# Kernel optimization log

Measured on AMD Instinct MI355X. Metric: run time of the kernel, lower is better.

## Reference

```python
import jax, jax.numpy as jnp
import numpy as np

B, T, C, H = 4096, 128, 128, 64  # T must equal BLOCK_SIZE=128, C=EMBEDDING_DIM=128


def setup_inputs() -> dict:
    key = jax.random.key(0)
    k1, k2, k3, k4, k5, k6 = jax.random.split(key, 6)
    source_embedding = jax.random.normal(k1, (B, T, C), dtype=jnp.float32)
    target_embedding = jax.random.normal(k2, (B, T, C), dtype=jnp.float32)
    # realistic padding: positions < length are valid; guarantees col 0 valid (no NaN rows)
    lengths = jax.random.randint(k3, (B,), 1, T + 1)
    pad_mask = jnp.arange(T)[None, :] < lengths[:, None]  # (B, T) bool
    Wq = jax.random.normal(k4, (C, H), dtype=jnp.float32) * 0.02
    Wk = jax.random.normal(k5, (C, H), dtype=jnp.float32) * 0.02
    Wv = jax.random.normal(k6, (C, H), dtype=jnp.float32) * 0.02
    return {"source_embedding": source_embedding, "target_embedding": target_embedding,
            "pad_mask": pad_mask, "Wq": Wq, "Wk": Wk, "Wv": Wv}


def reference(source_embedding, target_embedding, pad_mask, Wq, Wk, Wv):
    # q from target, k/v from source (cross-attention capable), bias-free projections
    q = target_embedding @ Wq   # (B, T, H)
    k = source_embedding @ Wk   # (B, T, H)
    v = source_embedding @ Wv   # (B, T, H)
    scale = k.shape[-1] ** -0.5
    wei = jnp.einsum('btd,bsd->bts', q, k) * scale  # (B, T, T)
    causal = jnp.tril(jnp.ones((T, T), dtype=bool))  # needs_future_mask=True
    mask = pad_mask[:, None, :] & causal[None, :, :]  # fuse pad + future masks
    wei = jnp.where(mask, wei, -jnp.inf)
    wei = jax.nn.softmax(wei, axis=-1)
    # dropout disabled (eval mode) for deterministic reference
    out = wei @ v  # (B, T, H)
    return out
```

## Files before the change

kernel.cpp:

```cpp
#include <hip/hip_runtime.h>
#include <stdint.h>


typedef uint32_t u32x2 __attribute__((ext_vector_type(2)));
typedef uint32_t u32x4 __attribute__((ext_vector_type(4)));
typedef float    f32x4 __attribute__((ext_vector_type(4)));
typedef __bf16   bf16x8 __attribute__((ext_vector_type(8)));

static __device__ __forceinline__ uint32_t pack2(float a, float b) {
  uint32_t ua = __builtin_bit_cast(uint32_t, a);
  uint32_t ub = __builtin_bit_cast(uint32_t, b);
  ua += 0x7FFFu + ((ua >> 16) & 1u);
  ub += 0x7FFFu + ((ub >> 16) & 1u);
  return (ua >> 16) | (ub & 0xFFFF0000u);
}
static __device__ __forceinline__ uint32_t cvt2(float a, float b) {
  uint16_t lo = __builtin_bit_cast(uint16_t, (__bf16)a);
  uint16_t hi = __builtin_bit_cast(uint16_t, (__bf16)b);
  return (uint32_t)lo | ((uint32_t)hi << 16);
}
static __device__ __forceinline__ f32x4 mfma16(u32x4 a, u32x4 b, f32x4 c) {
  return __builtin_amdgcn_mfma_f32_16x16x32_bf16(
      __builtin_bit_cast(bf16x8, a), __builtin_bit_cast(bf16x8, b), c, 0, 0, 0);
}

__global__ void prep_w(const float* __restrict__ Wq, const float* __restrict__ Wk,
                       const float* __restrict__ Wv, const void* __restrict__ mask,
                       uint32_t* __restrict__ ws) {
  const int blk = blockIdx.x;
  const int l = threadIdx.x;
  if (blk < 48) {
    const int m  = blk >> 4;
    const int ct = (blk >> 2) & 3;
    const int ks = blk & 3;
    const float* W = (m == 0) ? Wq : ((m == 1) ? Wk : Wv);
    const int h  = ct * 16 + (l & 15);
    const int c0 = ks * 32 + (l >> 4) * 8;
    u32x4 v;
#pragma unroll
    for (int p = 0; p < 4; ++p)
      v[p] = pack2(W[(c0 + 2 * p) * 64 + h], W[(c0 + 2 * p + 1) * 64 + h]);
    ((u32x4*)ws)[blk * 64 + l] = v;
  } else {
    const uint32_t* mw = (const uint32_t*)mask;
    int fl = 0;
    for (int i = l * 16; i < l * 16 + 16; ++i) {
      uint32_t x = mw[i];
      if (x == 0x3F800000u) fl = 2;
      else if (x > 1u && fl != 2) fl = 1;
    }
#pragma unroll
    for (int off = 32; off > 0; off >>= 1) {
      int o = __shfl_down(fl, off);
      fl = (o > fl) ? o : fl;
    }
    if (l == 0) ws[12288] = (uint32_t)fl;
  }
}

__global__ __launch_bounds__(512, 3) void attn_fused(
    const float* __restrict__ src, const float* __restrict__ tgt,
    const void* __restrict__ mask, const uint32_t* __restrict__ ws,
    float* __restrict__ out) {
  __shared__ __align__(16) uint8_t lds[49664];
  uint8_t* const EMB = lds;
  uint8_t* const Kb  = lds + 16384;
  uint8_t* const Vb  = lds + 32768;
  float*  const BIAS = (float*)(lds + 49152);

  const int b   = blockIdx.x;
  const int tid = (int)threadIdx.x;
  const int l   = tid & 63;
  const int w   = tid >> 6;
  const int l15 = l & 15;
  const int g4  = l >> 4;
  const int ct  = w & 3;
  const int sg  = (w >> 2) * 2;
  const int tq  = 16 * w + l15;

  const u32x4* wsv = (const u32x4*)ws;
  const int mflag = (int)ws[12288];
  const float* const srcb = src + (size_t)b * 16384;
  const float* const tgtb = tgt + (size_t)b * 16384;

  f32x4 qv[8];
  {
    const float* pq = tgtb + tq * 128 + g4 * 8;
#pragma unroll
    for (int ks = 0; ks < 4; ++ks) {
      qv[2 * ks]     = *(const f32x4*)(pq + ks * 32);
      qv[2 * ks + 1] = *(const f32x4*)(pq + ks * 32 + 4);
    }
  }
  f32x4 pf[4];
  auto stage_load = [&](const float* gbase) {
#pragma unroll
    for (int p = 0; p < 4; ++p)
      pf[p] = *(const f32x4*)(gbase + tid * 4 + p * 2048);
  };
  stage_load(srcb);
  float biasv = 0.0f;
  if (tid < 128) {
    bool valid;
    if (mflag == 1)      valid = ((const uint8_t*)mask)[b * 128 + tid] != 0;
    else if (mflag == 0) valid = ((const int*)mask)[b * 128 + tid] != 0;
    else                 valid = ((const float*)mask)[b * 128 + tid] != 0.0f;
    biasv = valid ? 0.0f : -1e30f;
  }

  uint32_t qp[8];
  {
    f32x4 c0 = {0,0,0,0}, c1 = {0,0,0,0}, c2 = {0,0,0,0}, c3 = {0,0,0,0};
#pragma unroll
    for (int ks = 0; ks < 4; ++ks) {
      u32x4 e = { cvt2(qv[2*ks][0], qv[2*ks][1]), cvt2(qv[2*ks][2], qv[2*ks][3]),
                  cvt2(qv[2*ks+1][0], qv[2*ks+1][1]), cvt2(qv[2*ks+1][2], qv[2*ks+1][3]) };
      c0 = mfma16(wsv[(0  + ks) * 64 + l], e, c0);
      c1 = mfma16(wsv[(4  + ks) * 64 + l], e, c1);
      c2 = mfma16(wsv[(8  + ks) * 64 + l], e, c2);
      c3 = mfma16(wsv[(12 + ks) * 64 + l], e, c3);
    }
    qp[0] = cvt2(c0[0], c0[1]); qp[1] = cvt2(c0[2], c0[3]);
    qp[2] = cvt2(c1[0], c1[1]); qp[3] = cvt2(c1[2], c1[3]);
    qp[4] = cvt2(c2[0], c2[1]); qp[5] = cvt2(c2[2], c2[3]);
    qp[6] = cvt2(c3[0], c3[1]); qp[7] = cvt2(c3[2], c3[3]);
  }

  auto stage_write = [&]() {
#pragma unroll
    for (int p = 0; p < 4; ++p) {
      const int c   = tid + p * 512;
      const int row = c >> 5;
      const int cc  = c & 31;
      u32x2 d = { cvt2(pf[p][0], pf[p][1]), cvt2(pf[p][2], pf[p][3]) };
      *(u32x2*)(EMB + (row << 8) + ((((cc >> 1) ^ (row & 7))) << 4) + ((cc & 1) << 3)) = d;
    }
  };
  u32x4 wk[4], wv[4];
#pragma unroll
  for (int ks = 0; ks < 4; ++ks) {
    wk[ks] = wsv[((4 + ct) * 4 + ks) * 64 + l];
    wv[ks] = wsv[((8 + ct) * 4 + ks) * 64 + l];
  }
  auto projKV = [&](int half) {
#pragma unroll
    for (int i = 0; i < 2; ++i) {
      const int st  = sg + i;
      const int row = st * 16 + l15;
      f32x4 cK = {0, 0, 0, 0}, cV = {0, 0, 0, 0};
#pragma unroll
      for (int ks = 0; ks < 4; ++ks) {
        u32x4 e = *(const u32x4*)(EMB + (row << 8) + ((((ks * 4 + g4) ^ (row & 7))) << 4));
        cK = mfma16(wk[ks], e, cK);
        cV = mfma16(e, wv[ks], cV);
      }
      const int s  = half * 64 + st * 16 + l15;
      const int h0 = ct * 16 + g4 * 4;
      u32x2 dk = { cvt2(cK[0], cK[1]), cvt2(cK[2], cK[3]) };
      *(u32x2*)(Kb + (s << 7) + ((((h0 >> 3) ^ (s & 7))) << 4) + ((h0 & 7) << 1)) = dk;
      const int s0 = half * 64 + st * 16 + g4 * 4;
      const int h  = ct * 16 + l15;
      u32x2 dv = { cvt2(cV[0], cV[1]), cvt2(cV[2], cV[3]) };
      *(u32x2*)(Vb + (h << 8) + ((((s0 >> 3) ^ (h & 7))) << 4) + ((s0 & 7) << 1)) = dv;
    }
  };

  stage_write();
  if (tid < 128) BIAS[tid] = biasv;
  __syncthreads();
  stage_load(srcb + 8192);
  projKV(0);
  __syncthreads();
  stage_write();
  __syncthreads();
  projKV(1);
  __syncthreads();

  uint8_t* const Qw = EMB + (w << 11) + (l15 << 7);
#pragma unroll
  for (int ctq = 0; ctq < 4; ++ctq) {
    u32x2 dq = { qp[2 * ctq], qp[2 * ctq + 1] };
    const int cw = ctq * 2 + (g4 >> 1);
    *(u32x2*)(Qw + (((cw ^ (l15 & 7))) << 4) + ((g4 & 1) << 3)) = dq;
  }
  u32x4 qB[2];
#pragma unroll
  for (int ks = 0; ks < 2; ++ks)
    qB[ks] = *(const u32x4*)(Qw + ((((ks * 4 + g4) ^ (l15 & 7))) << 4));

  f32x4 sacc[8];
#pragma unroll
  for (int mt = 0; mt < 8; ++mt) sacc[mt] = {0, 0, 0, 0};
  __builtin_amdgcn_s_setprio(1);
#pragma unroll
  for (int mt = 0; mt < 8; ++mt) {
    const int srow = mt * 16 + l15;
    u32x4 k0 = *(const u32x4*)(Kb + (srow << 7) + (((g4 ^ (srow & 7))) << 4));
    u32x4 k1 = *(const u32x4*)(Kb + (srow << 7) + ((((4 + g4) ^ (srow & 7))) << 4));
    sacc[mt] = mfma16(k0, qB[0], sacc[mt]);
    sacc[mt] = mfma16(k1, qB[1], sacc[mt]);
  }
  __builtin_amdgcn_s_setprio(0);

  __syncthreads();

  float m = -3.0e38f;
#pragma unroll
  for (int mt = 0; mt < 8; ++mt) {
    f32x4 b4 = *(const f32x4*)(BIAS + mt * 16 + g4 * 4);
#pragma unroll
    for (int r = 0; r < 4; ++r) {
      float v = sacc[mt][r] * 0.125f + b4[r];
      sacc[mt][r] = v;
      m = fmaxf(m, v);
    }
  }
  m = fmaxf(m, __shfl_xor(m, 16));
  m = fmaxf(m, __shfl_xor(m, 32));
  float sum = 0.0f;
#pragma unroll
  for (int mt = 0; mt < 8; ++mt) {
#pragma unroll
    for (int r = 0; r < 4; ++r) {
      const int s = mt * 16 + g4 * 4 + r;
      float p = __expf(sacc[mt][r] - m);
      p = (s <= tq) ? p : 0.0f;
      sacc[mt][r] = p;
      sum += p;
    }
  }
  sum += __shfl_xor(sum, 16);
  sum += __shfl_xor(sum, 32);
  const float inv = 1.0f / sum;

  uint8_t* const Pr = (l15 < 8) ? (EMB + (w << 11) + (l15 << 8))
                                : (Kb + (w << 11) + ((l15 - 8) << 8));
#pragma unroll
  for (int mt = 0; mt < 8; ++mt) {
    u32x2 d = { cvt2(sacc[mt][0], sacc[mt][1]), cvt2(sacc[mt][2], sacc[mt][3]) };
    const int c = mt * 2 + (g4 >> 1);
    *(u32x2*)(Pr + (((c ^ l15)) << 4) + ((g4 & 1) << 3)) = d;
  }

  f32x4 oacc[4];
#pragma unroll
  for (int vt = 0; vt < 4; ++vt) oacc[vt] = {0, 0, 0, 0};
  __builtin_amdgcn_s_setprio(1);
#pragma unroll
  for (int ks = 0; ks < 4; ++ks) {
    u32x4 pb = *(const u32x4*)(Pr + ((((ks * 4 + g4) ^ l15)) << 4));
#pragma unroll
    for (int vt = 0; vt < 4; ++vt) {
      const int vrow = vt * 16 + l15;
      u32x4 vf = *(const u32x4*)(Vb + (vrow << 8) + ((((ks * 4 + g4) ^ (vrow & 7))) << 4));
      oacc[vt] = mfma16(vf, pb, oacc[vt]);
    }
  }
  __builtin_amdgcn_s_setprio(0);

  float* const ob = out + (size_t)b * 8192 + (size_t)tq * 64;
#pragma unroll
  for (int vt = 0; vt < 4; ++vt) {
    f32x4 o = { oacc[vt][0] * inv, oacc[vt][1] * inv,
                oacc[vt][2] * inv, oacc[vt][3] * inv };
    *(f32x4*)(ob + vt * 16 + g4 * 4) = o;
  }
}

extern "C" void kernel_launch(void* const* d_in, const int* in_sizes, int n_in,
                              void* d_out, int out_size, void* d_ws, size_t ws_size,
                              hipStream_t stream) {
  const float* src = (const float*)d_in[0];
  const float* tgt = (const float*)d_in[1];
  const void*  msk = d_in[2];
  const float* Wq  = (const float*)d_in[3];
  const float* Wk  = (const float*)d_in[4];
  const float* Wv  = (const float*)d_in[5];
  uint32_t* ws = (uint32_t*)d_ws;
  float* out = (float*)d_out;
  const int B = in_sizes[0] / (128 * 128);

  hipLaunchKernelGGL(prep_w, dim3(49), dim3(64), 0, stream, Wq, Wk, Wv, msk, ws);
  hipLaunchKernelGGL(attn_fused, dim3(B), dim3(512), 0, stream,
                     src, tgt, msk, ws, out);
}
```

Before: 150.6 us.

## Process multiple batches per block with prefetch of next batch's inputs

Each block now loops over four batch elements instead of one, and prefetches the next element's Q rows, first source half and mask bias into registers during the softmax and PV phase of the current one. The goal is to hide global load latency across iterations and amortize block launch overhead. In exchange the grid shrinks to a quarter, launch bounds drop from 3 to 2 blocks per CU, register pressure rises from the prefetch buffers, and an extra barrier is added per iteration.

```diff
diff --git a/kernel.cpp b/kernel.cpp
--- a/kernel.cpp
+++ b/kernel.cpp
@@ -6,6 +6,8 @@
 typedef uint32_t u32x4 __attribute__((ext_vector_type(4)));
 typedef float    f32x4 __attribute__((ext_vector_type(4)));
 typedef __bf16   bf16x8 __attribute__((ext_vector_type(8)));
+
+#define NBATCH 4
 
 static __device__ __forceinline__ uint32_t pack2(float a, float b) {
   uint32_t ua = __builtin_bit_cast(uint32_t, a);
@@ -58,17 +60,16 @@
   }
 }
 
-__global__ __launch_bounds__(512, 3) void attn_fused(
+__global__ __launch_bounds__(512, 2) void attn_fused(
     const float* __restrict__ src, const float* __restrict__ tgt,
     const void* __restrict__ mask, const uint32_t* __restrict__ ws,
-    float* __restrict__ out) {
+    float* __restrict__ out, int Btot) {
   __shared__ __align__(16) uint8_t lds[49664];
   uint8_t* const EMB = lds;
   uint8_t* const Kb  = lds + 16384;
   uint8_t* const Vb  = lds + 32768;
   float*  const BIAS = (float*)(lds + 49152);
 
-  const int b   = blockIdx.x;
   const int tid = (int)threadIdx.x;
   const int l   = tid & 63;
   const int w   = tid >> 6;
@@ -80,52 +81,34 @@
 
   const u32x4* wsv = (const u32x4*)ws;
   const int mflag = (int)ws[12288];
-  const float* const srcb = src + (size_t)b * 16384;
-  const float* const tgtb = tgt + (size_t)b * 16384;
+
+  int b = blockIdx.x * NBATCH;
 
   f32x4 qv[8];
-  {
-    const float* pq = tgtb + tq * 128 + g4 * 8;
+  f32x4 pf[4];
+  float biasv;
+
+  auto load_q = [&](int bb) {
+    const float* pq = tgt + (size_t)bb * 16384 + tq * 128 + g4 * 8;
 #pragma unroll
     for (int ks = 0; ks < 4; ++ks) {
       qv[2 * ks]     = *(const f32x4*)(pq + ks * 32);
       qv[2 * ks + 1] = *(const f32x4*)(pq + ks * 32 + 4);
     }
-  }
-  f32x4 pf[4];
+  };
   auto stage_load = [&](const float* gbase) {
 #pragma unroll
     for (int p = 0; p < 4; ++p)
       pf[p] = *(const f32x4*)(gbase + tid * 4 + p * 2048);
   };
-  stage_load(srcb);
-  float biasv = 0.0f;
-  if (tid < 128) {
+  auto load_bias = [&](int bb) -> float {
+    if (tid >= 128) return 0.0f;
     bool valid;
-    if (mflag == 1)      valid = ((const uint8_t*)mask)[b * 128 + tid] != 0;
-    else if (mflag == 0) valid = ((const int*)mask)[b * 128 + tid] != 0;
-    else                 valid = ((const float*)mask)[b * 128 + tid] != 0.0f;
-    biasv = valid ? 0.0f : -1e30f;
-  }
-
-  uint32_t qp[8];
-  {
-    f32x4 c0 = {0,0,0,0}, c1 = {0,0,0,0}, c2 = {0,0,0,0}, c3 = {0,0,0,0};
-#pragma unroll
-    for (int ks = 0; ks < 4; ++ks) {
-      u32x4 e = { cvt2(qv[2*ks][0], qv[2*ks][1]), cvt2(qv[2*ks][2], qv[2*ks][3]),
-                  cvt2(qv[2*ks+1][0], qv[2*ks+1][1]), cvt2(qv[2*ks+1][2], qv[2*ks+1][3]) };
-      c0 = mfma16(wsv[(0  + ks) * 64 + l], e, c0);
-      c1 = mfma16(wsv[(4  + ks) * 64 + l], e, c1);
-      c2 = mfma16(wsv[(8  + ks) * 64 + l], e, c2);
-      c3 = mfma16(wsv[(12 + ks) * 64 + l], e, c3);
-    }
-    qp[0] = cvt2(c0[0], c0[1]); qp[1] = cvt2(c0[2], c0[3]);
-    qp[2] = cvt2(c1[0], c1[1]); qp[3] = cvt2(c1[2], c1[3]);
-    qp[4] = cvt2(c2[0], c2[1]); qp[5] = cvt2(c2[2], c2[3]);
-    qp[6] = cvt2(c3[0], c3[1]); qp[7] = cvt2(c3[2], c3[3]);
-  }
-
+    if (mflag == 1)      valid = ((const uint8_t*)mask)[bb * 128 + tid] != 0;
+    else if (mflag == 0) valid = ((const int*)mask)[bb * 128 + tid] != 0;
+    else                 valid = ((const float*)mask)[bb * 128 + tid] != 0.0f;
+    return valid ? 0.0f : -1e30f;
+  };
   auto stage_write = [&]() {
 #pragma unroll
     for (int p = 0; p < 4; ++p) {
@@ -136,12 +119,8 @@
       *(u32x2*)(EMB + (row << 8) + ((((cc >> 1) ^ (row & 7))) << 4) + ((cc & 1) << 3)) = d;
     }
   };
+
   u32x4 wk[4], wv[4];
-#pragma unroll
-  for (int ks = 0; ks < 4; ++ks) {
-    wk[ks] = wsv[((4 + ct) * 4 + ks) * 64 + l];
-    wv[ks] = wsv[((8 + ct) * 4 + ks) * 64 + l];
-  }
   auto projKV = [&](int half) {
 #pragma unroll
     for (int i = 0; i < 2; ++i) {
@@ -165,105 +144,147 @@
     }
   };
 
-  stage_write();
-  if (tid < 128) BIAS[tid] = biasv;
-  __syncthreads();
-  stage_load(srcb + 8192);
-  projKV(0);
-  __syncthreads();
-  stage_write();
-  __syncthreads();
-  projKV(1);
-  __syncthreads();
-
-  uint8_t* const Qw = EMB + (w << 11) + (l15 << 7);
-#pragma unroll
-  for (int ctq = 0; ctq < 4; ++ctq) {
-    u32x2 dq = { qp[2 * ctq], qp[2 * ctq + 1] };
-    const int cw = ctq * 2 + (g4 >> 1);
-    *(u32x2*)(Qw + (((cw ^ (l15 & 7))) << 4) + ((g4 & 1) << 3)) = dq;
-  }
-  u32x4 qB[2];
-#pragma unroll
-  for (int ks = 0; ks < 2; ++ks)
-    qB[ks] = *(const u32x4*)(Qw + ((((ks * 4 + g4) ^ (l15 & 7))) << 4));
-
-  f32x4 sacc[8];
-#pragma unroll
-  for (int mt = 0; mt < 8; ++mt) sacc[mt] = {0, 0, 0, 0};
-  __builtin_amdgcn_s_setprio(1);
-#pragma unroll
-  for (int mt = 0; mt < 8; ++mt) {
-    const int srow = mt * 16 + l15;
-    u32x4 k0 = *(const u32x4*)(Kb + (srow << 7) + (((g4 ^ (srow & 7))) << 4));
-    u32x4 k1 = *(const u32x4*)(Kb + (srow << 7) + ((((4 + g4) ^ (srow & 7))) << 4));
-    sacc[mt] = mfma16(k0, qB[0], sacc[mt]);
-    sacc[mt] = mfma16(k1, qB[1], sacc[mt]);
-  }
-  __builtin_amdgcn_s_setprio(0);
-
-  __syncthreads();
-
-  float m = -3.0e38f;
-#pragma unroll
-  for (int mt = 0; mt < 8; ++mt) {
-    f32x4 b4 = *(const f32x4*)(BIAS + mt * 16 + g4 * 4);
-#pragma unroll
-    for (int r = 0; r < 4; ++r) {
-      float v = sacc[mt][r] * 0.125f + b4[r];
-      sacc[mt][r] = v;
-      m = fmaxf(m, v);
-    }
-  }
-  m = fmaxf(m, __shfl_xor(m, 16));
-  m = fmaxf(m, __shfl_xor(m, 32));
-  float sum = 0.0f;
-#pragma unroll
-  for (int mt = 0; mt < 8; ++mt) {
-#pragma unroll
-    for (int r = 0; r < 4; ++r) {
-      const int s = mt * 16 + g4 * 4 + r;
-      float p = __expf(sacc[mt][r] - m);
-      p = (s <= tq) ? p : 0.0f;
-      sacc[mt][r] = p;
-      sum += p;
-    }
-  }
-  sum += __shfl_xor(sum, 16);
-  sum += __shfl_xor(sum, 32);
-  const float inv = 1.0f / sum;
-
-  uint8_t* const Pr = (l15 < 8) ? (EMB + (w << 11) + (l15 << 8))
-                                : (Kb + (w << 11) + ((l15 - 8) << 8));
-#pragma unroll
-  for (int mt = 0; mt < 8; ++mt) {
-    u32x2 d = { cvt2(sacc[mt][0], sacc[mt][1]), cvt2(sacc[mt][2], sacc[mt][3]) };
-    const int c = mt * 2 + (g4 >> 1);
-    *(u32x2*)(Pr + (((c ^ l15)) << 4) + ((g4 & 1) << 3)) = d;
-  }
-
-  f32x4 oacc[4];
-#pragma unroll
-  for (int vt = 0; vt < 4; ++vt) oacc[vt] = {0, 0, 0, 0};
-  __builtin_amdgcn_s_setprio(1);
-#pragma unroll
-  for (int ks = 0; ks < 4; ++ks) {
-    u32x4 pb = *(const u32x4*)(Pr + ((((ks * 4 + g4) ^ l15)) << 4));
+  load_q(b);
+  stage_load(src + (size_t)b * 16384);
+  biasv = load_bias(b);
+
+  for (int bi = 0; bi < NBATCH; ++bi) {
+    if (b >= Btot) break;
+    const float* const srcb = src + (size_t)b * 16384;
+
+#pragma unroll
+    for (int ks = 0; ks < 4; ++ks) {
+      wk[ks] = wsv[((4 + ct) * 4 + ks) * 64 + l];
+      wv[ks] = wsv[((8 + ct) * 4 + ks) * 64 + l];
+    }
+
+    uint32_t qp[8];
+    {
+      f32x4 c0 = {0,0,0,0}, c1 = {0,0,0,0}, c2 = {0,0,0,0}, c3 = {0,0,0,0};
+#pragma unroll
+      for (int ks = 0; ks < 4; ++ks) {
+        u32x4 e = { cvt2(qv[2*ks][0], qv[2*ks][1]), cvt2(qv[2*ks][2], qv[2*ks][3]),
+                    cvt2(qv[2*ks+1][0], qv[2*ks+1][1]), cvt2(qv[2*ks+1][2], qv[2*ks+1][3]) };
+        c0 = mfma16(wsv[(0  + ks) * 64 + l], e, c0);
+        c1 = mfma16(wsv[(4  + ks) * 64 + l], e, c1);
+        c2 = mfma16(wsv[(8  + ks) * 64 + l], e, c2);
+        c3 = mfma16(wsv[(12 + ks) * 64 + l], e, c3);
+      }
+      qp[0] = cvt2(c0[0], c0[1]); qp[1] = cvt2(c0[2], c0[3]);
+      qp[2] = cvt2(c1[0], c1[1]); qp[3] = cvt2(c1[2], c1[3]);
+      qp[4] = cvt2(c2[0], c2[1]); qp[5] = cvt2(c2[2], c2[3]);
+      qp[6] = cvt2(c3[0], c3[1]); qp[7] = cvt2(c3[2], c3[3]);
+    }
+
+    __syncthreads();
+    stage_write();
+    if (tid < 128) BIAS[tid] = biasv;
+    __syncthreads();
+    stage_load(srcb + 8192);
+    projKV(0);
+    __syncthreads();
+    stage_write();
+    __syncthreads();
+    projKV(1);
+    __syncthreads();
+
+    uint8_t* const Qw = EMB + (w << 11) + (l15 << 7);
+#pragma unroll
+    for (int ctq = 0; ctq < 4; ++ctq) {
+      u32x2 dq = { qp[2 * ctq], qp[2 * ctq + 1] };
+      const int cw = ctq * 2 + (g4 >> 1);
+      *(u32x2*)(Qw + (((cw ^ (l15 & 7))) << 4) + ((g4 & 1) << 3)) = dq;
+    }
+    u32x4 qB[2];
+#pragma unroll
+    for (int ks = 0; ks < 2; ++ks)
+      qB[ks] = *(const u32x4*)(Qw + ((((ks * 4 + g4) ^ (l15 & 7))) << 4));
+
+    f32x4 sacc[8];
+#pragma unroll
+    for (int mt = 0; mt < 8; ++mt) sacc[mt] = {0, 0, 0, 0};
+    __builtin_amdgcn_s_setprio(1);
+#pragma unroll
+    for (int mt = 0; mt < 8; ++mt) {
+      const int srow = mt * 16 + l15;
+      u32x4 k0 = *(const u32x4*)(Kb + (srow << 7) + (((g4 ^ (srow & 7))) << 4));
+      u32x4 k1 = *(const u32x4*)(Kb + (srow << 7) + ((((4 + g4) ^ (srow & 7))) << 4));
+      sacc[mt] = mfma16(k0, qB[0], sacc[mt]);
+      sacc[mt] = mfma16(k1, qB[1], sacc[mt]);
+    }
+    __builtin_amdgcn_s_setprio(0);
+
+    __syncthreads();
+
+    if (bi + 1 < NBATCH && b + 1 < Btot) {
+      load_q(b + 1);
+      stage_load(src + (size_t)(b + 1) * 16384);
+      biasv = load_bias(b + 1);
+    }
+
+    float m = -3.0e38f;
+#pragma unroll
+    for (int mt = 0; mt < 8; ++mt) {
+      f32x4 b4 = *(const f32x4*)(BIAS + mt * 16 + g4 * 4);
+#pragma unroll
+      for (int r = 0; r < 4; ++r) {
+        float v = sacc[mt][r] * 0.125f + b4[r];
+        sacc[mt][r] = v;
+        m = fmaxf(m, v);
+      }
+    }
+    m = fmaxf(m, __shfl_xor(m, 16));
+    m = fmaxf(m, __shfl_xor(m, 32));
+    float sum = 0.0f;
+#pragma unroll
+    for (int mt = 0; mt < 8; ++mt) {
+#pragma unroll
+      for (int r = 0; r < 4; ++r) {
+        const int s = mt * 16 + g4 * 4 + r;
+        float p = __expf(sacc[mt][r] - m);
+        p = (s <= tq) ? p : 0.0f;
+        sacc[mt][r] = p;
+        sum += p;
+      }
+    }
+    sum += __shfl_xor(sum, 16);
+    sum += __shfl_xor(sum, 32);
+    const float inv = 1.0f / sum;
+
+    uint8_t* const Pr = (l15 < 8) ? (EMB + (w << 11) + (l15 << 8))
+                                  : (Kb + (w << 11) + ((l15 - 8) << 8));
+#pragma unroll
+    for (int mt = 0; mt < 8; ++mt) {
+      u32x2 d = { cvt2(sacc[mt][0], sacc[mt][1]), cvt2(sacc[mt][2], sacc[mt][3]) };
+      const int c = mt * 2 + (g4 >> 1);
+      *(u32x2*)(Pr + (((c ^ l15)) << 4) + ((g4 & 1) << 3)) = d;
+    }
+
+    f32x4 oacc[4];
+#pragma unroll
+    for (int vt = 0; vt < 4; ++vt) oacc[vt] = {0, 0, 0, 0};
+    __builtin_amdgcn_s_setprio(1);
+#pragma unroll
+    for (int ks = 0; ks < 4; ++ks) {
+      u32x4 pb = *(const u32x4*)(Pr + ((((ks * 4 + g4) ^ l15)) << 4));
+#pragma unroll
+      for (int vt = 0; vt < 4; ++vt) {
+        const int vrow = vt * 16 + l15;
+        u32x4 vf = *(const u32x4*)(Vb + (vrow << 8) + ((((ks * 4 + g4) ^ (vrow & 7))) << 4));
+        oacc[vt] = mfma16(vf, pb, oacc[vt]);
+      }
+    }
+    __builtin_amdgcn_s_setprio(0);
+
+    float* const ob = out + (size_t)b * 8192 + (size_t)tq * 64;
 #pragma unroll
     for (int vt = 0; vt < 4; ++vt) {
-      const int vrow = vt * 16 + l15;
-      u32x4 vf = *(const u32x4*)(Vb + (vrow << 8) + ((((ks * 4 + g4) ^ (vrow & 7))) << 4));
-      oacc[vt] = mfma16(vf, pb, oacc[vt]);
-    }
-  }
-  __builtin_amdgcn_s_setprio(0);
-
-  float* const ob = out + (size_t)b * 8192 + (size_t)tq * 64;
-#pragma unroll
-  for (int vt = 0; vt < 4; ++vt) {
-    f32x4 o = { oacc[vt][0] * inv, oacc[vt][1] * inv,
-                oacc[vt][2] * inv, oacc[vt][3] * inv };
-    *(f32x4*)(ob + vt * 16 + g4 * 4) = o;
+      f32x4 o = { oacc[vt][0] * inv, oacc[vt][1] * inv,
+                  oacc[vt][2] * inv, oacc[vt][3] * inv };
+      *(f32x4*)(ob + vt * 16 + g4 * 4) = o;
+    }
+
+    ++b;
   }
 }
 
@@ -279,8 +300,9 @@
   uint32_t* ws = (uint32_t*)d_ws;
   float* out = (float*)d_out;
   const int B = in_sizes[0] / (128 * 128);
+  const int grid = (B + NBATCH - 1) / NBATCH;
 
   hipLaunchKernelGGL(prep_w, dim3(49), dim3(64), 0, stream, Wq, Wk, Wv, msk, ws);
-  hipLaunchKernelGGL(attn_fused, dim3(B), dim3(512), 0, stream,
-                     src, tgt, msk, ws, out);
-}
+  hipLaunchKernelGGL(attn_fused, dim3(grid), dim3(512), 0, stream,
+                     src, tgt, msk, ws, out, B);
+}
```

Measured after the change: 154.6 us. +2.7%, slower.
